# Performance work log

Measured on AMD Instinct MI355X. Metric: run time of the kernel, lower is better.

The kernel has to match this reference:

```python
import jax, jax.numpy as jnp
import numpy as np

RADIUS = 5.0
CORRECT_THRESHOLD = 0.5
NUM_CLASSES = 4
COORD_RANGE = 64.0  # keep coords in a small field so some preds actually match


def setup_inputs() -> dict:
    key = jax.random.key(0)
    k1, k2, k3, k4 = jax.random.split(key, 4)
    B, P, T = 16, 4096, 1024
    pred_cls = jax.random.randint(k1, (B, P, 1), 0, NUM_CLASSES).astype(jnp.float32)
    pred_xy = jax.random.uniform(k2, (B, P, 2), dtype=jnp.float32) * COORD_RANGE
    gt_cls = jax.random.randint(k3, (B, T, 1), 0, NUM_CLASSES).astype(jnp.float32)
    gt_xy = jax.random.uniform(k4, (B, T, 2), dtype=jnp.float32) * COORD_RANGE
    pred = jnp.concatenate([pred_cls, pred_xy], axis=-1)  # [B,P,3]
    gt = jnp.concatenate([gt_cls, gt_xy], axis=-1)        # [B,T,3]
    return {"pred": pred, "gt": gt}


def _radial_score(centers, targets):
    # centers: [B,P,2], targets: [B,T,2] -> [B,P,T]; sigmoid(1 - dist/radius)
    d = centers[:, :, None, :] - targets[:, None, :, :]
    dist = jnp.sqrt(jnp.sum(d * d, axis=-1))
    return jax.nn.sigmoid(1.0 - dist / RADIUS)


def reference(pred, gt):
    B, P, _ = pred.shape
    T = gt.shape[1]
    classes = pred[:, :, 0]          # [B,P]
    centers = pred[:, :, 1:3]        # [B,P,2]
    tclasses = gt[:, :, 0]           # [B,T]
    tcenters = gt[:, :, 1:3]         # [B,T,2]

    scores = _radial_score(centers, tcenters)                       # [B,P,T]
    valid = (scores >= CORRECT_THRESHOLD) & (
        classes[:, :, None] == tclasses[:, None, :])                # [B,P,T]

    # Greedy dedup (sort-by-score + unique on target col) keeps, per target,
    # its highest-scoring valid pred; the second unique (pred col) only drops
    # duplicate preds and never changes the set of matched pred indices.
    masked = jnp.where(valid, scores, -jnp.inf)
    best_pred = jnp.argmax(masked, axis=1)                          # [B,T]
    has_match = jnp.any(valid, axis=1)                              # [B,T]

    flat_idx = (best_pred + jnp.arange(B, dtype=best_pred.dtype)[:, None] * P).ravel()
    hits = jnp.zeros((B * P,), jnp.float32).at[flat_idx].add(
        has_match.ravel().astype(jnp.float32))
    correct = hits.reshape(B, P) > 0                                # [B,P]

    tp = correct.sum().astype(jnp.float32)
    fp = jnp.float32(B * P) - tp
    fn = jnp.float32(B * T) - tp

    eps = jnp.float32(1e-6)
    precision = (tp + eps) / (tp + eps + fp + eps)
    recall = (tp + eps) / (tp + fn + eps)
    f1 = 2.0 * precision * recall / (precision + recall)
    return 1.0 - f1
```

## Files before the change

### kernel.cpp

```cpp
#include <hip/hip_runtime.h>
#include <math.h>

#define BB 16
#define PP 4096
#define TT 1024
#define JT 16
#define QTR 1024
#define LIMKEY 0x41C80FFFu

__global__ __launch_bounds__(256) void match_kernel(const float* __restrict__ pred,
                                                    const float* __restrict__ gt,
                                                    unsigned* __restrict__ part) {
    const int blk   = blockIdx.x;
    const int b     = blk >> 6;
    const int ttile = (blk >> 2) & 15;
    const int qtr   = blk & 3;
    const int wave  = threadIdx.x >> 6;
    const int lane  = threadIdx.x & 63;
    const int tbase = ttile * 64 + wave * JT;
    const int pbase = qtr * QTR;

    const float* gb = gt + ((size_t)(b * TT + tbase)) * 3;
    float gx[JT], gy[JT];
    unsigned key[JT];
    #pragma unroll
    for (int j = 0; j < JT; ++j) {
        const float c = gb[j * 3 + 0];
        gx[j] = fmaf(c, 128.0f, gb[j * 3 + 1]);
        gy[j] = gb[j * 3 + 2];
        key[j] = 0xFFFFFFFFu;
    }

    const float* pl = pred + (size_t)b * PP * 3 + (size_t)(pbase + lane) * 3;

    #pragma unroll 4
    for (int i = 0; i < QTR / 64; ++i) {
        const float pc = pl[0];
        const float px = pl[1];
        const float py = pl[2];
        pl += 192;
        const float pxp = fmaf(pc, 128.0f, px);
        const unsigned po = (unsigned)(pbase + (i << 6) + lane);
        #pragma unroll
        for (int j = 0; j < JT; ++j) {
            const float dx = pxp - gx[j];
            const float dy = py - gy[j];
            const float d2 = fmaf(dx, dx, dy * dy);
            const unsigned kk = (__float_as_uint(d2) & 0xFFFFF000u) | po;
            key[j] = min(key[j], kk);
        }
    }

    for (int off = 32; off; off >>= 1) {
        #pragma unroll
        for (int j = 0; j < JT; ++j) {
            const unsigned o = __shfl_down(key[j], off, 64);
            key[j] = min(key[j], o);
        }
    }

    if (lane == 0) {
        #pragma unroll
        for (int j = 0; j < JT; ++j)
            part[(size_t)qtr * (BB * TT) + b * TT + tbase + j] = key[j];
    }
}

__global__ __launch_bounds__(1024) void tail_kernel(const unsigned* __restrict__ part,
                                                    float* __restrict__ out) {
    __shared__ unsigned bm[BB * PP / 32];
    for (int i = threadIdx.x; i < BB * PP / 32; i += 1024) bm[i] = 0;
    __syncthreads();

    #pragma unroll 4
    for (int i = threadIdx.x; i < BB * TT; i += 1024) {
        const unsigned k = min(min(part[i],               part[BB * TT + i]),
                               min(part[2 * BB * TT + i], part[3 * BB * TT + i]));
        if (k <= LIMKEY) {
            const unsigned g = (unsigned)(i >> 10) * PP + (k & 0xFFFu);
            atomicOr(&bm[g >> 5], 1u << (g & 31));
        }
    }
    __syncthreads();

    int sum = 0;
    for (int i = threadIdx.x; i < BB * PP / 32; i += 1024) sum += __popc(bm[i]);
    for (int off = 32; off; off >>= 1) sum += __shfl_down(sum, off, 64);

    __shared__ int ss[16];
    const int wid  = threadIdx.x >> 6;
    const int lane = threadIdx.x & 63;
    if (lane == 0) ss[wid] = sum;
    __syncthreads();
    if (threadIdx.x == 0) {
        int tp_i = 0;
        for (int w = 0; w < 16; ++w) tp_i += ss[w];
        const float tp = (float)tp_i;
        const float eps = 1e-6f;
        const float fp = (float)(BB * PP) - tp;
        const float fn = (float)(BB * TT) - tp;
        const float precision = (tp + eps) / (tp + eps + fp + eps);
        const float recall    = (tp + eps) / (tp + fn + eps);
        const float f1 = 2.0f * precision * recall / (precision + recall);
        out[0] = 1.0f - f1;
    }
}

extern "C" void kernel_launch(void* const* d_in, const int* in_sizes, int n_in,
                              void* d_out, int out_size, void* d_ws, size_t ws_size,
                              hipStream_t stream) {
    const float* pred = (const float*)d_in[0];
    const float* gt   = (const float*)d_in[1];
    float* out = (float*)d_out;
    unsigned* part = (unsigned*)d_ws;

    match_kernel<<<BB * 16 * 4, 256, 0, stream>>>(pred, gt, part);
    tail_kernel<<<1, 1024, 0, stream>>>(part, out);
}
```

Baseline: 72.31 us.

## Pre-transpose pred/gt into SoA with class-folded x for vectorized loads

Adds a transpose kernel that converts the AoS [cls,x,y] inputs into separate arrays of class-offset x and y. The match kernel then reads float4 vectors and handles four preds per lane per iteration. This replaces the strided 3-float scalar loads and the per-element fma. It costs an extra kernel launch, a workspace round-trip, and a changed assignment of pred indices to lanes.

```diff
diff --git a/kernel.cpp b/kernel.cpp
--- a/kernel.cpp
+++ b/kernel.cpp
@@ -8,8 +8,41 @@
 #define QTR 1024
 #define LIMKEY 0x41C80FFFu
 
-__global__ __launch_bounds__(256) void match_kernel(const float* __restrict__ pred,
-                                                    const float* __restrict__ gt,
+__global__ __launch_bounds__(256) void transpose_kernel(const float* __restrict__ pred,
+                                                        const float* __restrict__ gt,
+                                                        float* __restrict__ pred_xp,
+                                                        float* __restrict__ pred_y,
+                                                        float* __restrict__ tgt_xp,
+                                                        float* __restrict__ tgt_y) {
+    const int blk = blockIdx.x;
+    const float4* src;
+    float4* dxp; float4* dy;
+    int t;
+    if (blk < 64) {
+        t = blk * 256 + threadIdx.x;
+        src = (const float4*)pred;
+        dxp = (float4*)pred_xp; dy = (float4*)pred_y;
+    } else {
+        t = (blk - 64) * 256 + threadIdx.x;
+        src = (const float4*)gt;
+        dxp = (float4*)tgt_xp;  dy = (float4*)tgt_y;
+    }
+    const float4 v0 = src[3 * t + 0];
+    const float4 v1 = src[3 * t + 1];
+    const float4 v2 = src[3 * t + 2];
+    float4 xp, yy;
+    xp.x = fmaf(v0.x, 128.0f, v0.y);  yy.x = v0.z;
+    xp.y = fmaf(v0.w, 128.0f, v1.x);  yy.y = v1.y;
+    xp.z = fmaf(v1.z, 128.0f, v1.w);  yy.z = v2.x;
+    xp.w = fmaf(v2.y, 128.0f, v2.z);  yy.w = v2.w;
+    dxp[t] = xp;
+    dy[t]  = yy;
+}
+
+__global__ __launch_bounds__(256) void match_kernel(const float* __restrict__ pred_xp,
+                                                    const float* __restrict__ pred_y,
+                                                    const float* __restrict__ tgt_xp,
+                                                    const float* __restrict__ tgt_y,
                                                     unsigned* __restrict__ part) {
     const int blk   = blockIdx.x;
     const int b     = blk >> 6;
@@ -20,34 +53,45 @@
     const int tbase = ttile * 64 + wave * JT;
     const int pbase = qtr * QTR;
 
-    const float* gb = gt + ((size_t)(b * TT + tbase)) * 3;
     float gx[JT], gy[JT];
     unsigned key[JT];
+    {
+        const float4* gx4 = (const float4*)(tgt_xp + b * TT + tbase);
+        const float4* gy4 = (const float4*)(tgt_y  + b * TT + tbase);
+        #pragma unroll
+        for (int j4 = 0; j4 < JT / 4; ++j4) {
+            const float4 a = gx4[j4], c = gy4[j4];
+            gx[j4 * 4 + 0] = a.x; gx[j4 * 4 + 1] = a.y; gx[j4 * 4 + 2] = a.z; gx[j4 * 4 + 3] = a.w;
+            gy[j4 * 4 + 0] = c.x; gy[j4 * 4 + 1] = c.y; gy[j4 * 4 + 2] = c.z; gy[j4 * 4 + 3] = c.w;
+        }
+    }
     #pragma unroll
-    for (int j = 0; j < JT; ++j) {
-        const float c = gb[j * 3 + 0];
-        gx[j] = fmaf(c, 128.0f, gb[j * 3 + 1]);
-        gy[j] = gb[j * 3 + 2];
-        key[j] = 0xFFFFFFFFu;
-    }
+    for (int j = 0; j < JT; ++j) key[j] = 0xFFFFFFFFu;
 
-    const float* pl = pred + (size_t)b * PP * 3 + (size_t)(pbase + lane) * 3;
+    const float4* xp4 = (const float4*)(pred_xp + (size_t)b * PP + pbase);
+    const float4* yy4 = (const float4*)(pred_y  + (size_t)b * PP + pbase);
 
-    #pragma unroll 4
-    for (int i = 0; i < QTR / 64; ++i) {
-        const float pc = pl[0];
-        const float px = pl[1];
-        const float py = pl[2];
-        pl += 192;
-        const float pxp = fmaf(pc, 128.0f, px);
-        const unsigned po = (unsigned)(pbase + (i << 6) + lane);
+    #pragma unroll
+    for (int i = 0; i < QTR / 256; ++i) {
+        const int idx = i * 64 + lane;
+        const float4 xv = xp4[idx];
+        const float4 yv = yy4[idx];
+        const unsigned po0 = (unsigned)(pbase + idx * 4);
+        const float pxs[4] = {xv.x, xv.y, xv.z, xv.w};
+        const float pys[4] = {yv.x, yv.y, yv.z, yv.w};
         #pragma unroll
-        for (int j = 0; j < JT; ++j) {
-            const float dx = pxp - gx[j];
-            const float dy = py - gy[j];
-            const float d2 = fmaf(dx, dx, dy * dy);
-            const unsigned kk = (__float_as_uint(d2) & 0xFFFFF000u) | po;
-            key[j] = min(key[j], kk);
+        for (int k = 0; k < 4; ++k) {
+            const float px = pxs[k];
+            const float py = pys[k];
+            const unsigned po = po0 + k;
+            #pragma unroll
+            for (int j = 0; j < JT; ++j) {
+                const float dx = px - gx[j];
+                const float dy = py - gy[j];
+                const float d2 = fmaf(dx, dx, dy * dy);
+                const unsigned kk = (__float_as_uint(d2) & 0xFFFFF000u) | po;
+                key[j] = min(key[j], kk);
+            }
         }
     }
 
@@ -112,8 +156,15 @@
     const float* pred = (const float*)d_in[0];
     const float* gt   = (const float*)d_in[1];
     float* out = (float*)d_out;
-    unsigned* part = (unsigned*)d_ws;
 
-    match_kernel<<<BB * 16 * 4, 256, 0, stream>>>(pred, gt, part);
+    char* ws = (char*)d_ws;
+    float*    pred_xp = (float*)(ws + 0);
+    float*    pred_y  = (float*)(ws + 262144);
+    float*    tgt_xp  = (float*)(ws + 524288);
+    float*    tgt_y   = (float*)(ws + 589824);
+    unsigned* part    = (unsigned*)(ws + 655360);
+
+    transpose_kernel<<<80, 256, 0, stream>>>(pred, gt, pred_xp, pred_y, tgt_xp, tgt_y);
+    match_kernel<<<BB * 16 * 4, 256, 0, stream>>>(pred_xp, pred_y, tgt_xp, tgt_y, part);
     tail_kernel<<<1, 1024, 0, stream>>>(part, out);
 }
```

New measurement: 71.10 us. About the same (-1.7%).

## Replace brute-force pair search with spatial-grid bucketed neighbor search

Applied to the files above, without the earlier changes.

Adds a build kernel that bins predictions and targets by class and a 12x12 spatial grid (cell size 5.5, just above the match radius), producing CSR offsets with a shared-memory histogram and scan. The match kernel then has each target thread scan only the up-to-3x3 neighboring cells of its own class, instead of testing all 4096 predictions. This removes most of the O(P*T) distance work. In exchange it adds an extra kernel launch, atomics and scans, and a divergent per-thread loop run by only 64 blocks, which may underuse the GPU.

```diff
diff --git a/kernel.cpp b/kernel.cpp
--- a/kernel.cpp
+++ b/kernel.cpp
@@ -4,66 +4,141 @@
 #define BB 16
 #define PP 4096
 #define TT 1024
-#define JT 16
-#define QTR 1024
+#define NC 12
+#define NCELL (NC * NC)
+#define NBUK (NCELL * 4)
+#define CSCALE 0.181818187f
 #define LIMKEY 0x41C80FFFu
 
-__global__ __launch_bounds__(256) void match_kernel(const float* __restrict__ pred,
-                                                    const float* __restrict__ gt,
+__global__ __launch_bounds__(1024) void build_kernel(const float* __restrict__ pred,
+                                                     const float* __restrict__ gt,
+                                                     float* __restrict__ sx,
+                                                     float* __restrict__ sy,
+                                                     unsigned* __restrict__ spo,
+                                                     float* __restrict__ tx,
+                                                     float* __restrict__ ty,
+                                                     unsigned* __restrict__ tinfo,
+                                                     unsigned* __restrict__ csr) {
+    __shared__ unsigned hist[NBUK], scn[NBUK], cur[NBUK];
+    const int tid = threadIdx.x;
+
+    if (blockIdx.x < 16) {
+        const int b = blockIdx.x;
+        if (tid < NBUK) hist[tid] = 0;
+        __syncthreads();
+
+        const float4* src = (const float4*)(pred + (size_t)b * PP * 3);
+        const float4 v0 = src[3 * tid + 0];
+        const float4 v1 = src[3 * tid + 1];
+        const float4 v2 = src[3 * tid + 2];
+        const float pc[4] = {v0.x, v0.w, v1.z, v2.y};
+        const float px[4] = {v0.y, v1.x, v1.w, v2.z};
+        const float py[4] = {v0.z, v1.y, v2.x, v2.w};
+        unsigned id[4];
+        #pragma unroll
+        for (int k = 0; k < 4; ++k) {
+            const unsigned cx = (unsigned)(px[k] * CSCALE);
+            const unsigned cy = (unsigned)(py[k] * CSCALE);
+            id[k] = (unsigned)pc[k] * NCELL + cx * NC + cy;
+            atomicAdd(&hist[id[k]], 1u);
+        }
+        __syncthreads();
+        if (tid < NBUK) scn[tid] = hist[tid];
+        __syncthreads();
+        for (unsigned d = 1; d < NBUK; d <<= 1) {
+            unsigned v = 0;
+            if (tid < NBUK) { v = scn[tid]; if (tid >= d) v += scn[tid - d]; }
+            __syncthreads();
+            if (tid < NBUK) scn[tid] = v;
+            __syncthreads();
+        }
+        if (tid < NBUK) {
+            const unsigned cnt = hist[tid];
+            const unsigned off = scn[tid] - cnt;
+            cur[tid] = off;
+            csr[b * NBUK + tid] = off | (cnt << 16);
+        }
+        __syncthreads();
+        #pragma unroll
+        for (int k = 0; k < 4; ++k) {
+            const unsigned pos = atomicAdd(&cur[id[k]], 1u);
+            sx[(size_t)b * PP + pos]  = px[k];
+            sy[(size_t)b * PP + pos]  = py[k];
+            spo[(size_t)b * PP + pos] = (unsigned)(tid * 4 + k);
+        }
+    } else {
+        const int b = blockIdx.x - 16;
+        if (tid < NBUK) hist[tid] = 0;
+        __syncthreads();
+
+        const float* g = gt + ((size_t)b * TT + tid) * 3;
+        const float c = g[0], x = g[1], y = g[2];
+        const unsigned cx = (unsigned)(x * CSCALE);
+        const unsigned cy = (unsigned)(y * CSCALE);
+        const unsigned cell = cx * NC + cy;
+        const unsigned id = (unsigned)c * NCELL + cell;
+        atomicAdd(&hist[id], 1u);
+        __syncthreads();
+        if (tid < NBUK) scn[tid] = hist[tid];
+        __syncthreads();
+        for (unsigned d = 1; d < NBUK; d <<= 1) {
+            unsigned v = 0;
+            if (tid < NBUK) { v = scn[tid]; if (tid >= d) v += scn[tid - d]; }
+            __syncthreads();
+            if (tid < NBUK) scn[tid] = v;
+            __syncthreads();
+        }
+        if (tid < NBUK) cur[tid] = scn[tid] - hist[tid];
+        __syncthreads();
+        const unsigned pos = atomicAdd(&cur[id], 1u);
+        tx[(size_t)b * TT + pos]    = x;
+        ty[(size_t)b * TT + pos]    = y;
+        tinfo[(size_t)b * TT + pos] = ((unsigned)c << 16) | cell;
+    }
+}
+
+__global__ __launch_bounds__(256) void match_kernel(const float* __restrict__ sx,
+                                                    const float* __restrict__ sy,
+                                                    const unsigned* __restrict__ spo,
+                                                    const float* __restrict__ tx,
+                                                    const float* __restrict__ ty,
+                                                    const unsigned* __restrict__ tinfo,
+                                                    const unsigned* __restrict__ csr,
                                                     unsigned* __restrict__ part) {
-    const int blk   = blockIdx.x;
-    const int b     = blk >> 6;
-    const int ttile = (blk >> 2) & 15;
-    const int qtr   = blk & 3;
-    const int wave  = threadIdx.x >> 6;
-    const int lane  = threadIdx.x & 63;
-    const int tbase = ttile * 64 + wave * JT;
-    const int pbase = qtr * QTR;
-
-    const float* gb = gt + ((size_t)(b * TT + tbase)) * 3;
-    float gx[JT], gy[JT];
-    unsigned key[JT];
-    #pragma unroll
-    for (int j = 0; j < JT; ++j) {
-        const float c = gb[j * 3 + 0];
-        gx[j] = fmaf(c, 128.0f, gb[j * 3 + 1]);
-        gy[j] = gb[j * 3 + 2];
-        key[j] = 0xFFFFFFFFu;
-    }
-
-    const float* pl = pred + (size_t)b * PP * 3 + (size_t)(pbase + lane) * 3;
-
-    #pragma unroll 4
-    for (int i = 0; i < QTR / 64; ++i) {
-        const float pc = pl[0];
-        const float px = pl[1];
-        const float py = pl[2];
-        pl += 192;
-        const float pxp = fmaf(pc, 128.0f, px);
-        const unsigned po = (unsigned)(pbase + (i << 6) + lane);
-        #pragma unroll
-        for (int j = 0; j < JT; ++j) {
-            const float dx = pxp - gx[j];
-            const float dy = py - gy[j];
-            const float d2 = fmaf(dx, dx, dy * dy);
-            const unsigned kk = (__float_as_uint(d2) & 0xFFFFF000u) | po;
-            key[j] = min(key[j], kk);
-        }
-    }
-
-    for (int off = 32; off; off >>= 1) {
-        #pragma unroll
-        for (int j = 0; j < JT; ++j) {
-            const unsigned o = __shfl_down(key[j], off, 64);
-            key[j] = min(key[j], o);
-        }
-    }
-
-    if (lane == 0) {
-        #pragma unroll
-        for (int j = 0; j < JT; ++j)
-            part[(size_t)qtr * (BB * TT) + b * TT + tbase + j] = key[j];
-    }
+    const int b = blockIdx.x >> 2;
+    const int i = ((blockIdx.x & 3) << 8) + threadIdx.x;
+
+    const unsigned info = tinfo[(size_t)b * TT + i];
+    const unsigned cls  = info >> 16;
+    const unsigned cell = info & 0xFFFFu;
+    const float x = tx[(size_t)b * TT + i];
+    const float y = ty[(size_t)b * TT + i];
+
+    const unsigned cx = (cell * 5462u) >> 16;
+    const unsigned cy = cell - cx * NC;
+    const int x0 = cx ? -1 : 0, x1 = (cx < NC - 1) ? 1 : 0;
+    const int y0 = cy ? -1 : 0, y1 = (cy < NC - 1) ? 1 : 0;
+    const unsigned base = cls * NCELL + cell;
+    const unsigned* csrb = csr + b * NBUK;
+    const float* sxb = sx + (size_t)b * PP;
+    const float* syb = sy + (size_t)b * PP;
+    const unsigned* spob = spo + (size_t)b * PP;
+
+    unsigned best = 0xFFFFFFFFu;
+    for (int dx = x0; dx <= x1; ++dx) {
+        const unsigned w0 = csrb[(int)base + dx * NC + y0];
+        const unsigned w2 = csrb[(int)base + dx * NC + y1];
+        unsigned s = w0 & 0xFFFFu;
+        const unsigned e = (w2 & 0xFFFFu) + (w2 >> 16);
+        for (; s < e; ++s) {
+            const float ddx = sxb[s] - x;
+            const float ddy = syb[s] - y;
+            const float d2 = fmaf(ddx, ddx, ddy * ddy);
+            const unsigned kk = (__float_as_uint(d2) & 0xFFFFF000u) | spob[s];
+            best = min(best, kk);
+        }
+    }
+    part[(size_t)b * TT + i] = best;
 }
 
 __global__ __launch_bounds__(1024) void tail_kernel(const unsigned* __restrict__ part,
@@ -74,8 +149,7 @@
 
     #pragma unroll 4
     for (int i = threadIdx.x; i < BB * TT; i += 1024) {
-        const unsigned k = min(min(part[i],               part[BB * TT + i]),
-                               min(part[2 * BB * TT + i], part[3 * BB * TT + i]));
+        const unsigned k = part[i];
         if (k <= LIMKEY) {
             const unsigned g = (unsigned)(i >> 10) * PP + (k & 0xFFFu);
             atomicOr(&bm[g >> 5], 1u << (g & 31));
@@ -112,8 +186,18 @@
     const float* pred = (const float*)d_in[0];
     const float* gt   = (const float*)d_in[1];
     float* out = (float*)d_out;
-    unsigned* part = (unsigned*)d_ws;
-
-    match_kernel<<<BB * 16 * 4, 256, 0, stream>>>(pred, gt, part);
+
+    char* ws = (char*)d_ws;
+    float*    sx    = (float*)   (ws + 0);
+    float*    sy    = (float*)   (ws + 262144);
+    unsigned* spo   = (unsigned*)(ws + 524288);
+    float*    tx    = (float*)   (ws + 786432);
+    float*    ty    = (float*)   (ws + 851968);
+    unsigned* tinfo = (unsigned*)(ws + 917504);
+    unsigned* csr   = (unsigned*)(ws + 983040);
+    unsigned* part  = (unsigned*)(ws + 1019904);
+
+    build_kernel<<<32, 1024, 0, stream>>>(pred, gt, sx, sy, spo, tx, ty, tinfo, csr);
+    match_kernel<<<64, 256, 0, stream>>>(sx, sy, spo, tx, ty, tinfo, csr, part);
     tail_kernel<<<1, 1024, 0, stream>>>(part, out);
 }
```

New measurement: 79.26 us. 1.1x slower.
